# Performance work log

Hardware: AMD Instinct MI355X
Metric: run time of the kernel (lower is better)

## Reference

```python
import jax, jax.numpy as jnp
import numpy as np

EMBED_DIM = 1024
NUM_HEADS = 16
HEAD_DIM = EMBED_DIM // NUM_HEADS


def setup_inputs() -> dict:
    key = jax.random.key(0)
    k_x, k_wqkv, k_bqkv, k_wo, k_bo = jax.random.split(key, 5)
    B, T, C = 4, 2048, EMBED_DIM
    # PyTorch Linear default init scale ~ 1/sqrt(fan_in); use small normals
    s = 1.0 / np.sqrt(C)
    return {
        "x": jax.random.normal(k_x, (B, T, C), dtype=jnp.float32),
        "w_qkv": jax.random.normal(k_wqkv, (C, 3 * C), dtype=jnp.float32) * s,
        "b_qkv": jax.random.normal(k_bqkv, (3 * C,), dtype=jnp.float32) * s,
        "w_out": jax.random.normal(k_wo, (C, C), dtype=jnp.float32) * s,
        "b_out": jax.random.normal(k_bo, (C,), dtype=jnp.float32) * s,
    }


def reference(x, w_qkv, b_qkv, w_out, b_out):
    B, T, C = x.shape
    H, D = NUM_HEADS, HEAD_DIM
    qkv = x @ w_qkv + b_qkv                      # (B, T, 3C)
    q, k, v = jnp.split(qkv, 3, axis=-1)
    # (B, H, T, D)
    q = q.reshape(B, T, H, D).transpose(0, 2, 1, 3)
    k = k.reshape(B, T, H, D).transpose(0, 2, 1, 3)
    v = v.reshape(B, T, H, D).transpose(0, 2, 1, 3)
    scores = jnp.einsum("bhqd,bhkd->bhqk", q, k) / jnp.sqrt(jnp.float32(D))
    causal = jnp.tril(jnp.ones((T, T), dtype=bool))  # (T, T)
    scores = jnp.where(causal[None, None, :, :], scores, -jnp.inf)
    attn = jax.nn.softmax(scores, axis=-1)
    out = jnp.einsum("bhqk,bhkd->bhqd", attn, v)  # (B, H, T, D)
    out = out.transpose(0, 2, 1, 3).reshape(B, T, C)
    return out @ w_out + b_out
```

## Files before the change

kernel.cpp:

```cpp
#include <hip/hip_runtime.h>
#include <hip/hip_bf16.h>

#define B_  4
#define T_  2048
#define C_  1024
#define H_  16
#define D_  64
#define BH_ (B_*H_)

typedef float  f32x4  __attribute__((ext_vector_type(4)));
typedef __bf16 bf16x8 __attribute__((ext_vector_type(8)));
typedef __bf16 bf16x2 __attribute__((ext_vector_type(2)));

static __device__ __forceinline__ ushort f2bf(float f) {
    union { float f; unsigned u; } x; x.f = f;
    unsigned r = ((x.u >> 16) & 1u) + 0x7fffu;
    return (ushort)((x.u + r) >> 16);
}

static __device__ __forceinline__ uint packbf(float a, float b) {
    bf16x2 v = { (__bf16)a, (__bf16)b };
    return __builtin_bit_cast(uint, v);
}

static __device__ __forceinline__ void gload_lds16(const void* g, void* l) {
    __builtin_amdgcn_global_load_lds(
        (const __attribute__((address_space(1))) unsigned int*)g,
        (__attribute__((address_space(3))) unsigned int*)l, 16, 0, 0);
}

__global__ void cvt_kernel(const float* __restrict__ in, ushort* __restrict__ out, int n) {
    int i = (blockIdx.x * blockDim.x + threadIdx.x) * 4;
    if (i < n) {
        float4 v = *(const float4*)(in + i);
        ushort4 o;
        o.x = f2bf(v.x); o.y = f2bf(v.y); o.z = f2bf(v.z); o.w = f2bf(v.w);
        *(ushort4*)(out + i) = o;
    }
}

__global__ void transpose_cvt_kernel(const float* __restrict__ in, ushort* __restrict__ out,
                                     int K, int N) {
    __shared__ float tile[32][33];
    int k0 = blockIdx.y * 32, n0 = blockIdx.x * 32;
    int tx = threadIdx.x & 31, ty = threadIdx.x >> 5;
    #pragma unroll
    for (int r = 0; r < 32; r += 8)
        tile[ty + r][tx] = in[(size_t)(k0 + ty + r) * N + n0 + tx];
    __syncthreads();
    #pragma unroll
    for (int r = 0; r < 32; r += 8)
        out[(size_t)(n0 + ty + r) * K + k0 + tx] = f2bf(tile[tx][ty + r]);
}

__global__ void transpose_v_kernel(const ushort* __restrict__ v, ushort* __restrict__ vt) {
    __shared__ ushort tile[64][66];
    int bh = blockIdx.x >> 5;
    int t0 = (blockIdx.x & 31) * 64;
    const ushort* src = v  + ((size_t)bh * T_ + t0) * D_;
    ushort*       dst = vt + (size_t)bh * D_ * T_ + t0;
    int tx = threadIdx.x & 63, ty = threadIdx.x >> 6;
    #pragma unroll
    for (int r = 0; r < 64; r += 4)
        tile[ty + r][tx] = src[(size_t)(ty + r) * D_ + tx];
    __syncthreads();
    #pragma unroll
    for (int r = 0; r < 64; r += 4)
        dst[(size_t)(ty + r) * T_ + tx] = tile[tx][ty + r];
}

__global__ __launch_bounds__(256) void gemm_qkv_kernel(
    const ushort* __restrict__ A,
    const ushort* __restrict__ Bt,
    const float*  __restrict__ bias,
    ushort* __restrict__ qkv)
{
    constexpr int K = 1024;
    __shared__ __align__(16) ushort sA[128 * 64];
    __shared__ __align__(16) ushort sB[128 * 64];
    const int m0 = blockIdx.y * 128, n0 = blockIdx.x * 128;
    const int lane = threadIdx.x & 63, wv = threadIdx.x >> 6;
    const int wm = wv >> 1, wn = wv & 1;
    const int lr = lane & 15, lh = lane >> 4;
    f32x4 acc[4][4] = {};

    for (int kt = 0; kt < K; kt += 64) {
        #pragma unroll
        for (int i = 0; i < 4; ++i) {
            int j = i * 4 + wv;
            int p = j * 64 + lane;
            int row = p >> 3, kc = (p & 7) << 3;
            gload_lds16(A  + (size_t)(m0 + row) * K + kt + kc, &sA[j * 512]);
            gload_lds16(Bt + (size_t)(n0 + row) * K + kt + kc, &sB[j * 512]);
        }
        __syncthreads();
        #pragma unroll
        for (int ks = 0; ks < 2; ++ks) {
            bf16x8 af[4], bfr[4];
            #pragma unroll
            for (int mi = 0; mi < 4; ++mi)
                af[mi] = *(const bf16x8*)&sA[(wm * 64 + mi * 16 + lr) * 64 + ks * 32 + lh * 8];
            #pragma unroll
            for (int ni = 0; ni < 4; ++ni)
                bfr[ni] = *(const bf16x8*)&sB[(wn * 64 + ni * 16 + lr) * 64 + ks * 32 + lh * 8];
            #pragma unroll
            for (int mi = 0; mi < 4; ++mi)
                #pragma unroll
                for (int ni = 0; ni < 4; ++ni)
                    acc[mi][ni] = __builtin_amdgcn_mfma_f32_16x16x32_bf16(af[mi], bfr[ni], acc[mi][ni], 0, 0, 0);
        }
        __syncthreads();
    }

    #pragma unroll
    for (int mi = 0; mi < 4; ++mi) {
        #pragma unroll
        for (int ni = 0; ni < 4; ++ni) {
            int col = n0 + wn * 64 + ni * 16 + lr;
            float bv = bias[col];
            int which = col >> 10;
            int h = (col & 1023) >> 6;
            int d = col & 63;
            #pragma unroll
            for (int r = 0; r < 4; ++r) {
                int row = m0 + wm * 64 + mi * 16 + lh * 4 + r;
                int b = row >> 11, t = row & 2047;
                float v = acc[mi][ni][r] + bv;
                if (which == 0) v *= 0.18033688011112042f;
                qkv[(size_t)which * (BH_ * T_ * D_) +
                    (((size_t)(b * H_ + h)) * T_ + t) * D_ + d] = f2bf(v);
            }
        }
    }
}

__global__ __launch_bounds__(256, 4) void flash_kernel(
    const ushort* __restrict__ qb,
    const ushort* __restrict__ kb,
    const ushort* __restrict__ vt,
    ushort* __restrict__ ob)
{
    __shared__ __align__(16) ushort sK[2][64 * 64];
    __shared__ __align__(16) ushort sV[2][64 * 64];
    __shared__ __align__(16) ushort sP[4][16 * 64];
    const int bh  = blockIdx.x >> 4;
    const int pr  = blockIdx.x & 15;
    const int qtA = pr, qtB = 31 - pr;
    const int lane = threadIdx.x & 63, wv = threadIdx.x >> 6;
    const int lr = lane & 15, lh = lane >> 4;

    const ushort* qrowA = qb + ((size_t)bh * T_ + qtA * 64 + wv * 16 + lr) * D_;
    const ushort* qrowB = qb + ((size_t)bh * T_ + qtB * 64 + wv * 16 + lr) * D_;
    bf16x8 qfA0 = *(const bf16x8*)(qrowA + lh * 8);
    bf16x8 qfA1 = *(const bf16x8*)(qrowA + 32 + lh * 8);
    bf16x8 qfB0 = *(const bf16x8*)(qrowB + lh * 8);
    bf16x8 qfB1 = *(const bf16x8*)(qrowB + 32 + lh * 8);

    const int srow = lane >> 3;
    const int scol = ((lane & 7) ^ srow) * 8;
    const ushort* kbase = kb + (size_t)bh * T_ * D_;
    const ushort* vbase = vt + (size_t)bh * D_ * T_;

    const int sw   = (lr & 7) << 4;
    const int off0 = (16 * lh) ^ sw;
    const int off1 = (64 + 16 * lh) ^ sw;

    f32x4 oA[4] = {}, oB[4] = {};
    float mA = -1e30f, lA = 0.f, mB = -1e30f, lB = 0.f;

    auto redmax = [&](float x) {
        x = fmaxf(x, __int_as_float(__builtin_amdgcn_ds_swizzle(__float_as_int(x), 0x401F)));
        x = fmaxf(x, __shfl_xor(x, 32, 64));
        return x;
    };
    auto redsum = [&](float x) {
        x += __int_as_float(__builtin_amdgcn_ds_swizzle(__float_as_int(x), 0x401F));
        x += __shfl_xor(x, 32, 64);
        return x;
    };

    auto tile = [&](f32x4 (&o)[4], float& mrow, float& lsum,
                    const bf16x8& q0f, const bf16x8& q1f,
                    const char* K0, const char* V0, bool diag) {
        f32x4 s[4];
        __builtin_amdgcn_s_setprio(1);
        #pragma unroll
        for (int nt = 0; nt < 4; ++nt) {
            const char* krow = K0 + (nt * 16 + lr) * 128;
            bf16x8 k0 = *(const bf16x8*)(krow + off0);
            bf16x8 k1 = *(const bf16x8*)(krow + off1);
            f32x4 a = {0.f, 0.f, 0.f, 0.f};
            a = __builtin_amdgcn_mfma_f32_16x16x32_bf16(k0, q0f, a, 0, 0, 0);
            a = __builtin_amdgcn_mfma_f32_16x16x32_bf16(k1, q1f, a, 0, 0, 0);
            s[nt] = a;
        }
        __builtin_amdgcn_s_setprio(0);
        if (diag) {
            #pragma unroll
            for (int nt = 0; nt < 4; ++nt)
                #pragma unroll
                for (int r = 0; r < 4; ++r)
                    if (nt * 16 + lh * 4 + r > wv * 16 + lr) s[nt][r] = -INFINITY;
        }

        float pmax = fmaxf(fmaxf(fmaxf(s[0][0], s[0][1]), fmaxf(s[0][2], s[0][3])),
                           fmaxf(fmaxf(s[1][0], s[1][1]), fmaxf(s[1][2], s[1][3])));
        pmax = fmaxf(pmax, fmaxf(fmaxf(fmaxf(s[2][0], s[2][1]), fmaxf(s[2][2], s[2][3])),
                                 fmaxf(fmaxf(s[3][0], s[3][1]), fmaxf(s[3][2], s[3][3]))));
        pmax = redmax(pmax);

        if (__any(pmax > mrow + 8.f)) {
            float mnew = fmaxf(mrow, pmax);
            float al = __builtin_exp2f(mrow - mnew);
            lsum *= al;
            #pragma unroll
            for (int r = 0; r < 4; ++r) {
                float ar = __shfl(al, lh * 20 + r, 64);
                o[0][r] *= ar; o[1][r] *= ar; o[2][r] *= ar; o[3][r] *= ar;
            }
            mrow = mnew;
        }

        float rsum = 0.f;
        uint pk[8];
        #pragma unroll
        for (int nt = 0; nt < 4; ++nt) {
            float p0 = __builtin_exp2f(s[nt][0] - mrow);
            float p1 = __builtin_exp2f(s[nt][1] - mrow);
            float p2 = __builtin_exp2f(s[nt][2] - mrow);
            float p3 = __builtin_exp2f(s[nt][3] - mrow);
            rsum += (p0 + p1) + (p2 + p3);
            pk[nt * 2]     = packbf(p0, p1);
            pk[nt * 2 + 1] = packbf(p2, p3);
        }
        lsum += redsum(rsum);

        char* P = (char*)sP[wv];
        {
            char* prow = P + lr * 128;
            #pragma unroll
            for (int nt = 0; nt < 4; ++nt) {
                uint2 w; w.x = pk[nt * 2]; w.y = pk[nt * 2 + 1];
                *(uint2*)(prow + ((32 * nt + 8 * lh) ^ sw)) = w;
            }
        }
        asm volatile("" ::: "memory");
        bf16x8 pf0 = *(const bf16x8*)(P + lr * 128 + off0);
        bf16x8 pf1 = *(const bf16x8*)(P + lr * 128 + off1);

        __builtin_amdgcn_s_setprio(1);
        #pragma unroll
        for (int dt = 0; dt < 4; ++dt) {
            const char* vrow = V0 + (dt * 16 + lr) * 128;
            bf16x8 v0 = *(const bf16x8*)(vrow + off0);
            bf16x8 v1 = *(const bf16x8*)(vrow + off1);
            o[dt] = __builtin_amdgcn_mfma_f32_16x16x32_bf16(pf0, v0, o[dt], 0, 0, 0);
            o[dt] = __builtin_amdgcn_mfma_f32_16x16x32_bf16(pf1, v1, o[dt], 0, 0, 0);
        }
        __builtin_amdgcn_s_setprio(0);
    };

    #pragma unroll
    for (int i = 0; i < 2; ++i) {
        int j = i * 4 + wv;
        gload_lds16(kbase + (size_t)(j * 8 + srow) * D_ + scol, &sK[0][j * 512]);
        gload_lds16(vbase + (size_t)(j * 8 + srow) * T_ + scol, &sV[0][j * 512]);
    }
    __syncthreads();

    for (int kt = 0; kt <= qtB; ++kt) {
        const int cur = kt & 1;
        if (kt < qtB) {
            const int nb = cur ^ 1;
            #pragma unroll
            for (int i = 0; i < 2; ++i) {
                int j = i * 4 + wv;
                gload_lds16(kbase + (size_t)((kt + 1) * 64 + j * 8 + srow) * D_ + scol, &sK[nb][j * 512]);
                gload_lds16(vbase + (size_t)(j * 8 + srow) * T_ + (kt + 1) * 64 + scol, &sV[nb][j * 512]);
            }
        }
        const char* K0 = (const char*)sK[cur];
        const char* V0 = (const char*)sV[cur];
        if (kt <= qtA) tile(oA, mA, lA, qfA0, qfA1, K0, V0, kt == qtA);
        tile(oB, mB, lB, qfB0, qfB1, K0, V0, kt == qtB);
        __syncthreads();
    }

    const int b = bh >> 4, h = bh & 15;
    auto writeout = [&](f32x4 (&o)[4], float lsum, int q0) {
        float inv = 1.f / lsum;
        #pragma unroll
        for (int r = 0; r < 4; ++r) {
            float ir = __shfl(inv, lh * 20 + r, 64);
            int q = q0 + lh * 4 + r;
            #pragma unroll
            for (int dt = 0; dt < 4; ++dt)
                ob[((size_t)b * T_ + q) * C_ + h * 64 + dt * 16 + lr] = f2bf(o[dt][r] * ir);
        }
    };
    writeout(oA, lA, qtA * 64 + wv * 16);
    writeout(oB, lB, qtB * 64 + wv * 16);
}

__global__ __launch_bounds__(256) void gemm_out_kernel(
    const ushort* __restrict__ A,
    const ushort* __restrict__ Bt,
    const float*  __restrict__ bias,
    float* __restrict__ Cout)
{
    constexpr int K = 1024;
    __shared__ __align__(16) ushort sA[128 * 64];
    __shared__ __align__(16) ushort sB[128 * 64];
    const int m0 = blockIdx.y * 128, n0 = blockIdx.x * 128;
    const int lane = threadIdx.x & 63, wv = threadIdx.x >> 6;
    const int wm = wv >> 1, wn = wv & 1;
    const int lr = lane & 15, lh = lane >> 4;
    f32x4 acc[4][4] = {};

    for (int kt = 0; kt < K; kt += 64) {
        #pragma unroll
        for (int i = 0; i < 4; ++i) {
            int j = i * 4 + wv;
            int p = j * 64 + lane;
            int row = p >> 3, kc = (p & 7) << 3;
            gload_lds16(A  + (size_t)(m0 + row) * K + kt + kc, &sA[j * 512]);
            gload_lds16(Bt + (size_t)(n0 + row) * K + kt + kc, &sB[j * 512]);
        }
        __syncthreads();
        #pragma unroll
        for (int ks = 0; ks < 2; ++ks) {
            bf16x8 af[4], bfr[4];
            #pragma unroll
            for (int mi = 0; mi < 4; ++mi)
                af[mi] = *(const bf16x8*)&sA[(wm * 64 + mi * 16 + lr) * 64 + ks * 32 + lh * 8];
            #pragma unroll
            for (int ni = 0; ni < 4; ++ni)
                bfr[ni] = *(const bf16x8*)&sB[(wn * 64 + ni * 16 + lr) * 64 + ks * 32 + lh * 8];
            #pragma unroll
            for (int mi = 0; mi < 4; ++mi)
                #pragma unroll
                for (int ni = 0; ni < 4; ++ni)
                    acc[mi][ni] = __builtin_amdgcn_mfma_f32_16x16x32_bf16(af[mi], bfr[ni], acc[mi][ni], 0, 0, 0);
        }
        __syncthreads();
    }

    #pragma unroll
    for (int mi = 0; mi < 4; ++mi) {
        #pragma unroll
        for (int ni = 0; ni < 4; ++ni) {
            int col = n0 + wn * 64 + ni * 16 + lr;
            float bv = bias[col];
            #pragma unroll
            for (int r = 0; r < 4; ++r) {
                int row = m0 + wm * 64 + mi * 16 + lh * 4 + r;
                Cout[(size_t)row * C_ + col] = acc[mi][ni][r] + bv;
            }
        }
    }
}

extern "C" void kernel_launch(void* const* d_in, const int* in_sizes, int n_in,
                              void* d_out, int out_size, void* d_ws, size_t ws_size,
                              hipStream_t stream) {
    const float* x     = (const float*)d_in[0];
    const float* w_qkv = (const float*)d_in[1];
    const float* b_qkv = (const float*)d_in[2];
    const float* w_out = (const float*)d_in[3];
    const float* b_out = (const float*)d_in[4];
    float* out = (float*)d_out;

    char* ws = (char*)d_ws;
    ushort* xb     = (ushort*)(ws + 0);
    ushort* wqkvT  = (ushort*)(ws + 16777216);
    ushort* woutT  = (ushort*)(ws + 23068672);
    ushort* qkv    = (ushort*)(ws + 25165824);
    ushort* vT     = (ushort*)(ws + 75497472);
    ushort* attn   = xb;
    ushort* qb = qkv;
    ushort* kb = qkv + (size_t)BH_ * T_ * D_;
    ushort* vb = qkv + (size_t)2 * BH_ * T_ * D_;

    const int nx = B_ * T_ * C_;
    cvt_kernel<<<nx / 4 / 256, 256, 0, stream>>>(x, xb, nx);
    transpose_cvt_kernel<<<dim3(3 * C_ / 32, C_ / 32), 256, 0, stream>>>(w_qkv, wqkvT, C_, 3 * C_);
    transpose_cvt_kernel<<<dim3(C_ / 32, C_ / 32), 256, 0, stream>>>(w_out, woutT, C_, C_);
    gemm_qkv_kernel<<<dim3(3 * C_ / 128, B_ * T_ / 128), 256, 0, stream>>>(xb, wqkvT, b_qkv, qkv);
    transpose_v_kernel<<<BH_ * (T_ / 64), 256, 0, stream>>>(vb, vT);
    flash_kernel<<<BH_ * 16, 256, 0, stream>>>(qb, kb, vT, attn);
    gemm_out_kernel<<<dim3(C_ / 128, B_ * T_ / 128), 256, 0, stream>>>(attn, woutT, b_out, out);
}
```

Measured before the change: 215.4 us.

## Replace GEMMs with triple-buffered 512-thread kernel and interleave flash A/B tiles

Both projection GEMMs now use one templated 512-thread kernel. It has larger 256-wide N tiles, a three-slot LDS ring fed by direct global-to-LDS loads, explicit vmcnt waits, split-phase barriers and XOR-swizzled LDS reads. The aim is to overlap global loads with MFMA work and raise reuse per block. The flash kernel now computes the QK^T scores for both query tiles together, uses separate P buffers, and interleaves both tiles' PV MFMAs to expose more independent matrix work. This costs more registers and LDS, so occupancy falls (flash launch bounds drop from 4 to 3 blocks per CU) and the QKV GEMM grid shrinks.

```diff
diff --git a/kernel.cpp b/kernel.cpp
--- a/kernel.cpp
+++ b/kernel.cpp
@@ -27,6 +27,18 @@
     __builtin_amdgcn_global_load_lds(
         (const __attribute__((address_space(1))) unsigned int*)g,
         (__attribute__((address_space(3))) unsigned int*)l, 16, 0, 0);
+}
+
+template<int N> static __device__ __forceinline__ void waitcnt_vm() {
+    if constexpr (N == 0) asm volatile("s_waitcnt vmcnt(0)" ::: "memory");
+    else if constexpr (N == 3) asm volatile("s_waitcnt vmcnt(3)" ::: "memory");
+    else if constexpr (N == 4) asm volatile("s_waitcnt vmcnt(4)" ::: "memory");
+    else static_assert(N == 0 || N == 3 || N == 4);
+    __builtin_amdgcn_sched_barrier(0);
+}
+static __device__ __forceinline__ void lgkm0() {
+    asm volatile("s_waitcnt lgkmcnt(0)" ::: "memory");
+    __builtin_amdgcn_sched_barrier(0);
 }
 
 __global__ void cvt_kernel(const float* __restrict__ in, ushort* __restrict__ out, int n) {
@@ -69,72 +81,132 @@
         dst[(size_t)(ty + r) * T_ + tx] = tile[tx][ty + r];
 }
 
-__global__ __launch_bounds__(256) void gemm_qkv_kernel(
+template<int MF, bool QKV>
+__global__ __launch_bounds__(512, 2) void gemm8p_kernel(
     const ushort* __restrict__ A,
     const ushort* __restrict__ Bt,
     const float*  __restrict__ bias,
-    ushort* __restrict__ qkv)
+    void* __restrict__ outp)
 {
-    constexpr int K = 1024;
-    __shared__ __align__(16) ushort sA[128 * 64];
-    __shared__ __align__(16) ushort sB[128 * 64];
-    const int m0 = blockIdx.y * 128, n0 = blockIdx.x * 128;
-    const int lane = threadIdx.x & 63, wv = threadIdx.x >> 6;
-    const int wm = wv >> 1, wn = wv & 1;
+    constexpr int NT = 32;
+    constexpr int BM = MF * 32;
+    constexpr int APASS = BM / 128, BPASS = 2, P = APASS + BPASS;
+    constexpr int ASLOT = BM * 32;
+    constexpr int BSLOT = 256 * 32;
+    __shared__ __align__(16) ushort lds[3 * ASLOT + 3 * BSLOT];
+    ushort* sB0 = lds + 3 * ASLOT;
+
+    const int m0 = blockIdx.y * BM, n0 = blockIdx.x * 256;
+    const int tid = threadIdx.x, lane = tid & 63;
+    const int wv = tid >> 6, wm = wv >> 2, wn = wv & 3;
     const int lr = lane & 15, lh = lane >> 4;
-    f32x4 acc[4][4] = {};
-
-    for (int kt = 0; kt < K; kt += 64) {
-        #pragma unroll
-        for (int i = 0; i < 4; ++i) {
-            int j = i * 4 + wv;
-            int p = j * 64 + lane;
-            int row = p >> 3, kc = (p & 7) << 3;
-            gload_lds16(A  + (size_t)(m0 + row) * K + kt + kc, &sA[j * 512]);
-            gload_lds16(Bt + (size_t)(n0 + row) * K + kt + kc, &sB[j * 512]);
-        }
-        __syncthreads();
-        #pragma unroll
-        for (int ks = 0; ks < 2; ++ks) {
-            bf16x8 af[4], bfr[4];
-            #pragma unroll
-            for (int mi = 0; mi < 4; ++mi)
-                af[mi] = *(const bf16x8*)&sA[(wm * 64 + mi * 16 + lr) * 64 + ks * 32 + lh * 8];
-            #pragma unroll
-            for (int ni = 0; ni < 4; ++ni)
-                bfr[ni] = *(const bf16x8*)&sB[(wn * 64 + ni * 16 + lr) * 64 + ks * 32 + lh * 8];
-            #pragma unroll
-            for (int mi = 0; mi < 4; ++mi)
-                #pragma unroll
-                for (int ni = 0; ni < 4; ++ni)
-                    acc[mi][ni] = __builtin_amdgcn_mfma_f32_16x16x32_bf16(af[mi], bfr[ni], acc[mi][ni], 0, 0, 0);
-        }
-        __syncthreads();
+    const int cxor = (lr >> 1) & 3;
+
+    const int srow = tid >> 2;
+    const int sc = (tid & 3) ^ ((tid >> 3) & 3);
+    const ushort* Asrc = A  + (size_t)m0 * 1024 + sc * 8;
+    const ushort* Bsrc = Bt + (size_t)n0 * 1024 + sc * 8;
+
+    f32x4 acc[MF][4] = {};
+
+    auto stageA = [&](int t, int slot) {
+        #pragma unroll
+        for (int p = 0; p < APASS; ++p)
+            gload_lds16(Asrc + (size_t)(p * 128 + srow) * 1024 + t * 32,
+                        (char*)lds + slot * (ASLOT * 2) + p * 8192 + tid * 16);
+    };
+    auto stageB = [&](int t, int slot) {
+        #pragma unroll
+        for (int p = 0; p < BPASS; ++p)
+            gload_lds16(Bsrc + (size_t)(p * 128 + srow) * 1024 + t * 32,
+                        (char*)sB0 + slot * (BSLOT * 2) + p * 8192 + tid * 16);
+    };
+    auto readA = [&](bf16x8 (&af)[MF], int slot) {
+        const char* base = (const char*)lds + slot * (ASLOT * 2);
+        #pragma unroll
+        for (int mi = 0; mi < MF; ++mi) {
+            int row = wm * (MF * 16) + mi * 16 + lr;
+            af[mi] = *(const bf16x8*)(base + row * 64 + (lh ^ cxor) * 16);
+        }
+    };
+    auto readB2 = [&](bf16x8 (&bf)[2], int slot, int nh) {
+        const char* base = (const char*)sB0 + slot * (BSLOT * 2);
+        #pragma unroll
+        for (int i = 0; i < 2; ++i) {
+            int row = wn * 64 + nh * 32 + i * 16 + lr;
+            bf[i] = *(const bf16x8*)(base + row * 64 + (lh ^ cxor) * 16);
+        }
+    };
+
+    stageA(0, 0); stageB(0, 0);
+    stageA(1, 1); stageB(1, 1);
+    waitcnt_vm<P>();
+    __builtin_amdgcn_s_barrier();
+
+    int s0 = 0, s1 = 1, s2 = 2;
+    for (int t = 0; t < NT; ++t) {
+        bf16x8 af[MF], bf0[2], bf1[2];
+        readA(af, s0);
+        readB2(bf0, s0, 0);
+        if (t + 2 < NT) stageA(t + 2, s2);
+        __builtin_amdgcn_s_barrier();
+        lgkm0();
+        __builtin_amdgcn_s_setprio(1);
+        #pragma unroll
+        for (int mi = 0; mi < MF; ++mi) {
+            acc[mi][0] = __builtin_amdgcn_mfma_f32_16x16x32_bf16(af[mi], bf0[0], acc[mi][0], 0, 0, 0);
+            acc[mi][1] = __builtin_amdgcn_mfma_f32_16x16x32_bf16(af[mi], bf0[1], acc[mi][1], 0, 0, 0);
+        }
+        __builtin_amdgcn_s_setprio(0);
+        readB2(bf1, s0, 1);
+        if (t + 2 < NT) stageB(t + 2, s2);
+        if (t < NT - 2) waitcnt_vm<P>(); else waitcnt_vm<0>();
+        __builtin_amdgcn_s_barrier();
+        lgkm0();
+        __builtin_amdgcn_s_setprio(1);
+        #pragma unroll
+        for (int mi = 0; mi < MF; ++mi) {
+            acc[mi][2] = __builtin_amdgcn_mfma_f32_16x16x32_bf16(af[mi], bf1[0], acc[mi][2], 0, 0, 0);
+            acc[mi][3] = __builtin_amdgcn_mfma_f32_16x16x32_bf16(af[mi], bf1[1], acc[mi][3], 0, 0, 0);
+        }
+        __builtin_amdgcn_s_setprio(0);
+        __builtin_amdgcn_s_barrier();
+        int tmp = s0; s0 = s1; s1 = s2; s2 = tmp;
     }
 
     #pragma unroll
-    for (int mi = 0; mi < 4; ++mi) {
+    for (int mi = 0; mi < MF; ++mi) {
         #pragma unroll
         for (int ni = 0; ni < 4; ++ni) {
             int col = n0 + wn * 64 + ni * 16 + lr;
             float bv = bias[col];
-            int which = col >> 10;
-            int h = (col & 1023) >> 6;
-            int d = col & 63;
-            #pragma unroll
-            for (int r = 0; r < 4; ++r) {
-                int row = m0 + wm * 64 + mi * 16 + lh * 4 + r;
-                int b = row >> 11, t = row & 2047;
-                float v = acc[mi][ni][r] + bv;
-                if (which == 0) v *= 0.18033688011112042f;
-                qkv[(size_t)which * (BH_ * T_ * D_) +
-                    (((size_t)(b * H_ + h)) * T_ + t) * D_ + d] = f2bf(v);
+            if constexpr (QKV) {
+                ushort* qkv = (ushort*)outp;
+                int which = col >> 10;
+                int h = (col & 1023) >> 6;
+                int d = col & 63;
+                #pragma unroll
+                for (int r = 0; r < 4; ++r) {
+                    int row = m0 + wm * (MF * 16) + mi * 16 + lh * 4 + r;
+                    int b = row >> 11, t = row & 2047;
+                    float v = acc[mi][ni][r] + bv;
+                    if (which == 0) v *= 0.18033688011112042f;
+                    qkv[(size_t)which * (BH_ * T_ * D_) +
+                        (((size_t)(b * H_ + h)) * T_ + t) * D_ + d] = f2bf(v);
+                }
+            } else {
+                float* Cout = (float*)outp;
+                #pragma unroll
+                for (int r = 0; r < 4; ++r) {
+                    int row = m0 + wm * (MF * 16) + mi * 16 + lh * 4 + r;
+                    Cout[(size_t)row * C_ + col] = acc[mi][ni][r] + bv;
+                }
             }
         }
     }
 }
 
-__global__ __launch_bounds__(256, 4) void flash_kernel(
+__global__ __launch_bounds__(256, 3) void flash_kernel(
     const ushort* __restrict__ qb,
     const ushort* __restrict__ kb,
     const ushort* __restrict__ vt,
@@ -142,7 +214,7 @@
 {
     __shared__ __align__(16) ushort sK[2][64 * 64];
     __shared__ __align__(16) ushort sV[2][64 * 64];
-    __shared__ __align__(16) ushort sP[4][16 * 64];
+    __shared__ __align__(16) ushort sP[8][16 * 64];
     const int bh  = blockIdx.x >> 4;
     const int pr  = blockIdx.x & 15;
     const int qtA = pr, qtB = 31 - pr;
@@ -179,36 +251,12 @@
         return x;
     };
 
-    auto tile = [&](f32x4 (&o)[4], float& mrow, float& lsum,
-                    const bf16x8& q0f, const bf16x8& q1f,
-                    const char* K0, const char* V0, bool diag) {
-        f32x4 s[4];
-        __builtin_amdgcn_s_setprio(1);
-        #pragma unroll
-        for (int nt = 0; nt < 4; ++nt) {
-            const char* krow = K0 + (nt * 16 + lr) * 128;
-            bf16x8 k0 = *(const bf16x8*)(krow + off0);
-            bf16x8 k1 = *(const bf16x8*)(krow + off1);
-            f32x4 a = {0.f, 0.f, 0.f, 0.f};
-            a = __builtin_amdgcn_mfma_f32_16x16x32_bf16(k0, q0f, a, 0, 0, 0);
-            a = __builtin_amdgcn_mfma_f32_16x16x32_bf16(k1, q1f, a, 0, 0, 0);
-            s[nt] = a;
-        }
-        __builtin_amdgcn_s_setprio(0);
-        if (diag) {
-            #pragma unroll
-            for (int nt = 0; nt < 4; ++nt)
-                #pragma unroll
-                for (int r = 0; r < 4; ++r)
-                    if (nt * 16 + lh * 4 + r > wv * 16 + lr) s[nt][r] = -INFINITY;
-        }
-
+    auto softmax = [&](f32x4 (&s)[4], float& mrow, float& lsum, f32x4 (&o)[4], char* P) {
         float pmax = fmaxf(fmaxf(fmaxf(s[0][0], s[0][1]), fmaxf(s[0][2], s[0][3])),
                            fmaxf(fmaxf(s[1][0], s[1][1]), fmaxf(s[1][2], s[1][3])));
         pmax = fmaxf(pmax, fmaxf(fmaxf(fmaxf(s[2][0], s[2][1]), fmaxf(s[2][2], s[2][3])),
                                  fmaxf(fmaxf(s[3][0], s[3][1]), fmaxf(s[3][2], s[3][3]))));
         pmax = redmax(pmax);
-
         if (__any(pmax > mrow + 8.f)) {
             float mnew = fmaxf(mrow, pmax);
             float al = __builtin_exp2f(mrow - mnew);
@@ -220,7 +268,6 @@
             }
             mrow = mnew;
         }
-
         float rsum = 0.f;
         uint pk[8];
         #pragma unroll
@@ -234,30 +281,12 @@
             pk[nt * 2 + 1] = packbf(p2, p3);
         }
         lsum += redsum(rsum);
-
-        char* P = (char*)sP[wv];
-        {
-            char* prow = P + lr * 128;
-            #pragma unroll
-            for (int nt = 0; nt < 4; ++nt) {
-                uint2 w; w.x = pk[nt * 2]; w.y = pk[nt * 2 + 1];
-                *(uint2*)(prow + ((32 * nt + 8 * lh) ^ sw)) = w;
-            }
-        }
-        asm volatile("" ::: "memory");
-        bf16x8 pf0 = *(const bf16x8*)(P + lr * 128 + off0);
-        bf16x8 pf1 = *(const bf16x8*)(P + lr * 128 + off1);
-
-        __builtin_amdgcn_s_setprio(1);
-        #pragma unroll
-        for (int dt = 0; dt < 4; ++dt) {
-            const char* vrow = V0 + (dt * 16 + lr) * 128;
-            bf16x8 v0 = *(const bf16x8*)(vrow + off0);
-            bf16x8 v1 = *(const bf16x8*)(vrow + off1);
-            o[dt] = __builtin_amdgcn_mfma_f32_16x16x32_bf16(pf0, v0, o[dt], 0, 0, 0);
-            o[dt] = __builtin_amdgcn_mfma_f32_16x16x32_bf16(pf1, v1, o[dt], 0, 0, 0);
-        }
-        __builtin_amdgcn_s_setprio(0);
+        char* prow = P + lr * 128;
+        #pragma unroll
+        for (int nt = 0; nt < 4; ++nt) {
+            uint2 w; w.x = pk[nt * 2]; w.y = pk[nt * 2 + 1];
+            *(uint2*)(prow + ((32 * nt + 8 * lh) ^ sw)) = w;
+        }
     };
 
     #pragma unroll
@@ -279,10 +308,88 @@
                 gload_lds16(vbase + (size_t)(j * 8 + srow) * T_ + (kt + 1) * 64 + scol, &sV[nb][j * 512]);
             }
         }
+        const bool doA = kt <= qtA;
         const char* K0 = (const char*)sK[cur];
         const char* V0 = (const char*)sV[cur];
-        if (kt <= qtA) tile(oA, mA, lA, qfA0, qfA1, K0, V0, kt == qtA);
-        tile(oB, mB, lB, qfB0, qfB1, K0, V0, kt == qtB);
+
+        f32x4 sa[4], sb[4];
+        __builtin_amdgcn_s_setprio(1);
+        if (doA) {
+            #pragma unroll
+            for (int nt = 0; nt < 4; ++nt) {
+                const char* krow = K0 + (nt * 16 + lr) * 128;
+                bf16x8 k0 = *(const bf16x8*)(krow + off0);
+                bf16x8 k1 = *(const bf16x8*)(krow + off1);
+                f32x4 a = {0.f, 0.f, 0.f, 0.f};
+                a = __builtin_amdgcn_mfma_f32_16x16x32_bf16(k0, qfB0, a, 0, 0, 0);
+                a = __builtin_amdgcn_mfma_f32_16x16x32_bf16(k1, qfB1, a, 0, 0, 0);
+                sb[nt] = a;
+                f32x4 c = {0.f, 0.f, 0.f, 0.f};
+                c = __builtin_amdgcn_mfma_f32_16x16x32_bf16(k0, qfA0, c, 0, 0, 0);
+                c = __builtin_amdgcn_mfma_f32_16x16x32_bf16(k1, qfA1, c, 0, 0, 0);
+                sa[nt] = c;
+            }
+        } else {
+            #pragma unroll
+            for (int nt = 0; nt < 4; ++nt) {
+                const char* krow = K0 + (nt * 16 + lr) * 128;
+                bf16x8 k0 = *(const bf16x8*)(krow + off0);
+                bf16x8 k1 = *(const bf16x8*)(krow + off1);
+                f32x4 a = {0.f, 0.f, 0.f, 0.f};
+                a = __builtin_amdgcn_mfma_f32_16x16x32_bf16(k0, qfB0, a, 0, 0, 0);
+                a = __builtin_amdgcn_mfma_f32_16x16x32_bf16(k1, qfB1, a, 0, 0, 0);
+                sb[nt] = a;
+            }
+        }
+        __builtin_amdgcn_s_setprio(0);
+
+        if (kt == qtB) {
+            #pragma unroll
+            for (int nt = 0; nt < 4; ++nt)
+                #pragma unroll
+                for (int r = 0; r < 4; ++r)
+                    if (nt * 16 + lh * 4 + r > wv * 16 + lr) sb[nt][r] = -INFINITY;
+        }
+        if (doA && kt == qtA) {
+            #pragma unroll
+            for (int nt = 0; nt < 4; ++nt)
+                #pragma unroll
+                for (int r = 0; r < 4; ++r)
+                    if (nt * 16 + lh * 4 + r > wv * 16 + lr) sa[nt][r] = -INFINITY;
+        }
+
+        softmax(sb, mB, lB, oB, (char*)sP[wv]);
+        if (doA) softmax(sa, mA, lA, oA, (char*)sP[4 + wv]);
+        asm volatile("" ::: "memory");
+
+        bf16x8 pfB0 = *(const bf16x8*)((char*)sP[wv] + lr * 128 + off0);
+        bf16x8 pfB1 = *(const bf16x8*)((char*)sP[wv] + lr * 128 + off1);
+
+        __builtin_amdgcn_s_setprio(1);
+        if (doA) {
+            bf16x8 pfA0 = *(const bf16x8*)((char*)sP[4 + wv] + lr * 128 + off0);
+            bf16x8 pfA1 = *(const bf16x8*)((char*)sP[4 + wv] + lr * 128 + off1);
+            #pragma unroll
+            for (int dt = 0; dt < 4; ++dt) {
+                const char* vrow = V0 + (dt * 16 + lr) * 128;
+                bf16x8 v0 = *(const bf16x8*)(vrow + off0);
+                bf16x8 v1 = *(const bf16x8*)(vrow + off1);
+                oB[dt] = __builtin_amdgcn_mfma_f32_16x16x32_bf16(pfB0, v0, oB[dt], 0, 0, 0);
+                oB[dt] = __builtin_amdgcn_mfma_f32_16x16x32_bf16(pfB1, v1, oB[dt], 0, 0, 0);
+                oA[dt] = __builtin_amdgcn_mfma_f32_16x16x32_bf16(pfA0, v0, oA[dt], 0, 0, 0);
+                oA[dt] = __builtin_amdgcn_mfma_f32_16x16x32_bf16(pfA1, v1, oA[dt], 0, 0, 0);
+            }
+        } else {
+            #pragma unroll
+            for (int dt = 0; dt < 4; ++dt) {
+                const char* vrow = V0 + (dt * 16 + lr) * 128;
+                bf16x8 v0 = *(const bf16x8*)(vrow + off0);
+                bf16x8 v1 = *(const bf16x8*)(vrow + off1);
+                oB[dt] = __builtin_amdgcn_mfma_f32_16x16x32_bf16(pfB0, v0, oB[dt], 0, 0, 0);
+                oB[dt] = __builtin_amdgcn_mfma_f32_16x16x32_bf16(pfB1, v1, oB[dt], 0, 0, 0);
+            }
+        }
+        __builtin_amdgcn_s_setprio(0);
         __syncthreads();
     }
 
@@ -300,64 +407,6 @@
     };
     writeout(oA, lA, qtA * 64 + wv * 16);
     writeout(oB, lB, qtB * 64 + wv * 16);
-}
-
-__global__ __launch_bounds__(256) void gemm_out_kernel(
-    const ushort* __restrict__ A,
-    const ushort* __restrict__ Bt,
-    const float*  __restrict__ bias,
-    float* __restrict__ Cout)
-{
-    constexpr int K = 1024;
-    __shared__ __align__(16) ushort sA[128 * 64];
-    __shared__ __align__(16) ushort sB[128 * 64];
-    const int m0 = blockIdx.y * 128, n0 = blockIdx.x * 128;
-    const int lane = threadIdx.x & 63, wv = threadIdx.x >> 6;
-    const int wm = wv >> 1, wn = wv & 1;
-    const int lr = lane & 15, lh = lane >> 4;
-    f32x4 acc[4][4] = {};
-
-    for (int kt = 0; kt < K; kt += 64) {
-        #pragma unroll
-        for (int i = 0; i < 4; ++i) {
-            int j = i * 4 + wv;
-            int p = j * 64 + lane;
-            int row = p >> 3, kc = (p & 7) << 3;
-            gload_lds16(A  + (size_t)(m0 + row) * K + kt + kc, &sA[j * 512]);
-            gload_lds16(Bt + (size_t)(n0 + row) * K + kt + kc, &sB[j * 512]);
-        }
-        __syncthreads();
-        #pragma unroll
-        for (int ks = 0; ks < 2; ++ks) {
-            bf16x8 af[4], bfr[4];
-            #pragma unroll
-            for (int mi = 0; mi < 4; ++mi)
-                af[mi] = *(const bf16x8*)&sA[(wm * 64 + mi * 16 + lr) * 64 + ks * 32 + lh * 8];
-            #pragma unroll
-            for (int ni = 0; ni < 4; ++ni)
-                bfr[ni] = *(const bf16x8*)&sB[(wn * 64 + ni * 16 + lr) * 64 + ks * 32 + lh * 8];
-            #pragma unroll
-            for (int mi = 0; mi < 4; ++mi)
-                #pragma unroll
-                for (int ni = 0; ni < 4; ++ni)
-                    acc[mi][ni] = __builtin_amdgcn_mfma_f32_16x16x32_bf16(af[mi], bfr[ni], acc[mi][ni], 0, 0, 0);
-        }
-        __syncthreads();
-    }
-
-    #pragma unroll
-    for (int mi = 0; mi < 4; ++mi) {
-        #pragma unroll
-        for (int ni = 0; ni < 4; ++ni) {
-            int col = n0 + wn * 64 + ni * 16 + lr;
-            float bv = bias[col];
-            #pragma unroll
-            for (int r = 0; r < 4; ++r) {
-                int row = m0 + wm * 64 + mi * 16 + lh * 4 + r;
-                Cout[(size_t)row * C_ + col] = acc[mi][ni][r] + bv;
-            }
-        }
-    }
 }
 
 extern "C" void kernel_launch(void* const* d_in, const int* in_sizes, int n_in,
@@ -385,8 +434,8 @@
     cvt_kernel<<<nx / 4 / 256, 256, 0, stream>>>(x, xb, nx);
     transpose_cvt_kernel<<<dim3(3 * C_ / 32, C_ / 32), 256, 0, stream>>>(w_qkv, wqkvT, C_, 3 * C_);
     transpose_cvt_kernel<<<dim3(C_ / 32, C_ / 32), 256, 0, stream>>>(w_out, woutT, C_, C_);
-    gemm_qkv_kernel<<<dim3(3 * C_ / 128, B_ * T_ / 128), 256, 0, stream>>>(xb, wqkvT, b_qkv, qkv);
+    gemm8p_kernel<8, true><<<dim3(3 * C_ / 256, B_ * T_ / 256), 512, 0, stream>>>(xb, wqkvT, b_qkv, qkv);
     transpose_v_kernel<<<BH_ * (T_ / 64), 256, 0, stream>>>(vb, vT);
     flash_kernel<<<BH_ * 16, 256, 0, stream>>>(qb, kb, vT, attn);
-    gemm_out_kernel<<<dim3(C_ / 128, B_ * T_ / 128), 256, 0, stream>>>(attn, woutT, b_out, out);
-}
+    gemm8p_kernel<4, false><<<dim3(C_ / 256, B_ * T_ / 128), 512, 0, stream>>>(attn, woutT, b_out, out);
+}
```

Measured after the change: 226.7 us. 1.05x slower.
